# Performance work log

Measured on AMD Instinct MI355X. Metric: run time of the kernel, lower is better.

Reference implementation:

```python
import jax, jax.numpy as jnp
import numpy as np

D_MODEL, D_K, D_V, H = 64, 32, 32, 8
B, HH, WW = 2, 48, 48
NQ = HH * WW


def setup_inputs() -> dict:
    key = jax.random.key(0)
    ks = jax.random.split(key, 16)
    inp = {
        "queries": jax.random.normal(ks[0], (B, D_MODEL, HH, WW), jnp.float32),
        "keys": jax.random.normal(ks[1], (B, D_MODEL, HH, WW), jnp.float32),
        "values": jax.random.normal(ks[2], (B, D_MODEL, HH, WW), jnp.float32),
        "attention_weights": jax.random.uniform(ks[3], (B, H, NQ, NQ), jnp.float32),
        "attention_mask": jax.random.randint(ks[4], (B, H, NQ, NQ), 0, 2) > 0,
        # Linear params: torch init normal(std=0.001) weights, zero bias
        "Wq": 0.001 * jax.random.normal(ks[5], (H * D_K, D_MODEL), jnp.float32),
        "bq": jnp.zeros((H * D_K,), jnp.float32),
        "Wk": 0.001 * jax.random.normal(ks[6], (H * D_K, D_MODEL), jnp.float32),
        "bk": jnp.zeros((H * D_K,), jnp.float32),
        "Wv": 0.001 * jax.random.normal(ks[7], (H * D_V, D_MODEL), jnp.float32),
        "bv": jnp.zeros((H * D_V,), jnp.float32),
        "Wo": 0.001 * jax.random.normal(ks[8], (D_MODEL, H * D_V), jnp.float32),
        "bo": jnp.zeros((D_MODEL,), jnp.float32),
    }
    return inp


def reference(queries, keys, values, attention_weights, attention_mask,
              Wq, bq, Wk, bk, Wv, bv, Wo, bo):
    b, c, hh, ww = queries.shape
    nq = hh * ww
    # torch .view(b, -1, c) on contiguous (b,c,h,w) is a raw row-major reshape
    qf = queries.reshape(b, nq, c)
    kf = keys.reshape(b, nq, c)
    vf = values.reshape(b, nq, c)
    q = (qf @ Wq.T + bq).reshape(b, nq, H, D_K).transpose(0, 2, 1, 3)  # b h nq dk
    k = (kf @ Wk.T + bk).reshape(b, nq, H, D_K).transpose(0, 2, 1, 3)  # b h nk dk
    v = (vf @ Wv.T + bv).reshape(b, nq, H, D_V).transpose(0, 2, 1, 3)  # b h nk dv
    att = jnp.einsum('bhqd,bhkd->bhqk', q, k) / np.sqrt(D_K).astype(np.float32)
    att = att * attention_weights
    att = jnp.where(attention_mask, -jnp.inf, att)
    att = jax.nn.softmax(att, axis=-1)  # dropout is identity in eval mode
    out = jnp.einsum('bhqk,bhkd->bhqd', att, v)
    out = out.transpose(0, 2, 1, 3).reshape(b, nq, H * D_V)
    out = out @ Wo.T + bo  # (b, nq, d_model)
    return out.reshape(b, -1, hh, ww)  # (b, d_model, h, w)
```

## Files before the change

kernel.cpp:

```cpp
#include <hip/hip_runtime.h>


typedef __attribute__((ext_vector_type(8))) short bf16x8;
typedef __attribute__((ext_vector_type(4))) short bf16x4;
typedef __attribute__((ext_vector_type(4))) float f32x4;
typedef __attribute__((ext_vector_type(4))) unsigned int u32x4;

constexpr int B_  = 2;
constexpr int H_  = 8;
constexpr int NQ_ = 2304;
constexpr int DM_ = 64;
constexpr int DK_ = 32;
constexpr int NT_ = NQ_ / 32;
constexpr int CH_ = 3;
constexpr int TPC_ = NT_ / CH_;
constexpr int GT_ = B_ * H_ * (NQ_ / 16);
constexpr float SCALE_ = 0.17677669529663687f;

constexpr size_t OFF_Q    = 0;
constexpr size_t OFF_K    = 2359296;
constexpr size_t OFF_V    = 4718592;
constexpr size_t OFF_OMID = 7077888;
constexpr size_t OFF_FLAG = 11796480;
constexpr size_t OFF_OP   = 11796736;
constexpr size_t OFF_ML   = 25952512;

static __device__ __forceinline__ unsigned short f2bf(float f) {
    unsigned int u = __builtin_bit_cast(unsigned int, f);
    u += 0x7fffu + ((u >> 16) & 1u);
    return (unsigned short)(u >> 16);
}

__global__ void detect_mask_k(const unsigned int* __restrict__ m, int* __restrict__ flag) {
    int t = threadIdx.x;
    unsigned int v = 0;
    for (int k = 0; k < 16; ++k) v |= m[t * 16 + k];
    unsigned long long b = __ballot(v > 1u);
    if (t == 0) *flag = (b != 0ull) ? 1 : 0;
}

__global__ __launch_bounds__(256) void proj_qkv_k(
    const float* __restrict__ qin, const float* __restrict__ kin, const float* __restrict__ vin,
    const float* __restrict__ Wq, const float* __restrict__ bq,
    const float* __restrict__ Wk, const float* __restrict__ bk,
    const float* __restrict__ Wv, const float* __restrict__ bv,
    unsigned short* __restrict__ Qbf, unsigned short* __restrict__ Kbf,
    unsigned short* __restrict__ Vbf)
{
    const int sel = blockIdx.y;
    const float* in  = sel == 0 ? qin : (sel == 1 ? kin : vin);
    const float* W   = sel == 0 ? Wq  : (sel == 1 ? Wk  : Wv);
    const float* bia = sel == 0 ? bq  : (sel == 1 ? bk  : bv);

    const int rt = blockIdx.x;
    const int b  = rt / (NQ_ / 8);
    const int r0 = (rt % (NQ_ / 8)) * 8;

    __shared__ alignas(16) float ins[8][64];
    const int t = threadIdx.x;
    const float4* src = reinterpret_cast<const float4*>(in + ((size_t)b * NQ_ + r0) * DM_);
    if (t < 128) reinterpret_cast<float4*>(&ins[0][0])[t] = src[t];
    __syncthreads();

    float acc[8];
#pragma unroll
    for (int r = 0; r < 8; ++r) acc[r] = 0.f;
    const float* wrow = W + t * DM_;
    for (int m = 0; m < DM_; ++m) {
        float wv = wrow[m];
#pragma unroll
        for (int r = 0; r < 8; ++r) acc[r] += ins[r][m] * wv;
    }
    const float bb = bia[t];
    const int h = t >> 5, d = t & 31;
#pragma unroll
    for (int r = 0; r < 8; ++r) {
        unsigned short bvv = f2bf(acc[r] + bb);
        if (sel == 2) Vbf[(((size_t)b * H_ + h) * DK_ + d) * NQ_ + (r0 + r)] = bvv;
        else {
            unsigned short* out = (sel == 1) ? Kbf : Qbf;
            out[(((size_t)b * H_ + h) * NQ_ + (r0 + r)) * DK_ + d] = bvv;
        }
    }
}

__global__ __launch_bounds__(256) void attn_k(
    const unsigned short* __restrict__ Qbf,
    const unsigned short* __restrict__ Kbf,
    const unsigned short* __restrict__ Vbf,
    const float* __restrict__ attw,
    const unsigned char* __restrict__ maskb,
    const int* __restrict__ flagp,
    float* __restrict__ Opart,
    float* __restrict__ MLpart)
{
    const int lane = threadIdx.x & 63;
    const int l15 = lane & 15, hi = lane >> 4;
    const int g = blockIdx.x * 4 + (threadIdx.x >> 6);
    const int chunk = blockIdx.y;
    const int bh = g / (NQ_ / 16);
    const int it = g % (NQ_ / 16);
    const int i0 = it * 16;
    const bool isbyte = (*flagp) != 0;

    const unsigned short* qbase = Qbf + (size_t)bh * NQ_ * DK_;
    const unsigned short* kbase = Kbf + (size_t)bh * NQ_ * DK_;
    const unsigned short* vbase = Vbf + (size_t)bh * DK_ * NQ_;

    const int q = i0 + l15;
    bf16x8 qb = *reinterpret_cast<const bf16x8*>(qbase + (size_t)q * DK_ + 8 * hi);

    const float* wrow = attw + ((size_t)bh * NQ_ + q) * NQ_;
    const size_t mrow = ((size_t)bh * NQ_ + q) * NQ_;

    f32x4 oacc0 = {0.f, 0.f, 0.f, 0.f}, oacc1 = {0.f, 0.f, 0.f, 0.f};
    const f32x4 zero = {0.f, 0.f, 0.f, 0.f};
    float mrun = -1e30f, lrun = 0.f;

    const int t0 = chunk * TPC_, t1 = t0 + TPC_;
    for (int t = t0; t < t1; ++t) {
        const int j0 = t * 32;
        bf16x8 ka0 = *reinterpret_cast<const bf16x8*>(kbase + (size_t)(j0 + l15) * DK_ + 8 * hi);
        bf16x8 ka1 = *reinterpret_cast<const bf16x8*>(kbase + (size_t)(j0 + 16 + l15) * DK_ + 8 * hi);
        f32x4 s0 = __builtin_amdgcn_mfma_f32_16x16x32_bf16(ka0, qb, zero, 0, 0, 0);
        f32x4 s1 = __builtin_amdgcn_mfma_f32_16x16x32_bf16(ka1, qb, zero, 0, 0, 0);

        f32x4 w0 = *reinterpret_cast<const f32x4*>(wrow + j0 + 4 * hi);
        f32x4 w1 = *reinterpret_cast<const f32x4*>(wrow + j0 + 16 + 4 * hi);
        unsigned int ba, bb;
        if (isbyte) {
            ba = *reinterpret_cast<const unsigned int*>(maskb + mrow + j0 + 4 * hi);
            bb = *reinterpret_cast<const unsigned int*>(maskb + mrow + j0 + 16 + 4 * hi);
        } else {
            u32x4 A = *reinterpret_cast<const u32x4*>(maskb + (mrow + j0 + 4 * hi) * 4);
            u32x4 Bv = *reinterpret_cast<const u32x4*>(maskb + (mrow + j0 + 16 + 4 * hi) * 4);
            ba = (A[0] & 1u) | ((A[1] & 1u) << 8) | ((A[2] & 1u) << 16) | ((A[3] & 1u) << 24);
            bb = (Bv[0] & 1u) | ((Bv[1] & 1u) << 8) | ((Bv[2] & 1u) << 16) | ((Bv[3] & 1u) << 24);
        }

        float x0[4], x1[4];
#pragma unroll
        for (int r = 0; r < 4; ++r) {
            x0[r] = ((ba >> (8 * r)) & 0xffu) ? -1e30f : s0[r] * (SCALE_ * w0[r]);
            x1[r] = ((bb >> (8 * r)) & 0xffu) ? -1e30f : s1[r] * (SCALE_ * w1[r]);
        }

        float tm = fmaxf(fmaxf(fmaxf(x0[0], x0[1]), fmaxf(x0[2], x0[3])),
                         fmaxf(fmaxf(x1[0], x1[1]), fmaxf(x1[2], x1[3])));
        tm = fmaxf(tm, __shfl_xor(tm, 16, 64));
        tm = fmaxf(tm, __shfl_xor(tm, 32, 64));
        float mnew = fmaxf(mrun, tm);
        float rf = __expf(mrun - mnew);
        float p0[4], p1[4], ts = 0.f;
#pragma unroll
        for (int r = 0; r < 4; ++r) {
            p0[r] = __expf(x0[r] - mnew);
            p1[r] = __expf(x1[r] - mnew);
            ts += p0[r] + p1[r];
        }
        ts += __shfl_xor(ts, 16, 64);
        ts += __shfl_xor(ts, 32, 64);
        lrun = lrun * rf + ts;
        mrun = mnew;

#pragma unroll
        for (int r = 0; r < 4; ++r) {
            float rfr = __shfl(rf, 4 * hi + r, 64);
            oacc0[r] *= rfr;
            oacc1[r] *= rfr;
        }

        bf16x8 pa;
#pragma unroll
        for (int r = 0; r < 4; ++r) {
            pa[r]     = (short)f2bf(p0[r]);
            pa[4 + r] = (short)f2bf(p1[r]);
        }
        bf16x4 v00 = *reinterpret_cast<const bf16x4*>(vbase + (size_t)l15 * NQ_ + j0 + 4 * hi);
        bf16x4 v01 = *reinterpret_cast<const bf16x4*>(vbase + (size_t)l15 * NQ_ + j0 + 16 + 4 * hi);
        bf16x4 v10 = *reinterpret_cast<const bf16x4*>(vbase + (size_t)(16 + l15) * NQ_ + j0 + 4 * hi);
        bf16x4 v11 = *reinterpret_cast<const bf16x4*>(vbase + (size_t)(16 + l15) * NQ_ + j0 + 16 + 4 * hi);
        bf16x8 vb0 = __builtin_shufflevector(v00, v01, 0, 1, 2, 3, 4, 5, 6, 7);
        bf16x8 vb1 = __builtin_shufflevector(v10, v11, 0, 1, 2, 3, 4, 5, 6, 7);
        oacc0 = __builtin_amdgcn_mfma_f32_16x16x32_bf16(pa, vb0, oacc0, 0, 0, 0);
        oacc1 = __builtin_amdgcn_mfma_f32_16x16x32_bf16(pa, vb1, oacc1, 0, 0, 0);
    }

    float* op = Opart + ((size_t)chunk * GT_ + g) * 512;
#pragma unroll
    for (int r = 0; r < 4; ++r) {
        op[(4 * hi + r) * 32 + l15]      = oacc0[r];
        op[(4 * hi + r) * 32 + 16 + l15] = oacc1[r];
    }
    if (hi == 0) {
        float* mlp = MLpart + ((size_t)chunk * GT_ + g) * 32;
        mlp[l15]      = mrun;
        mlp[16 + l15] = lrun;
    }
}

__global__ __launch_bounds__(64) void combine_k(
    const float* __restrict__ Opart, const float* __restrict__ MLpart,
    float* __restrict__ Omid)
{
    const int g = blockIdx.x;
    const int lane = threadIdx.x;
    const int row = lane >> 2;
    const int c4  = (lane & 3) * 8;
    const int bh = g / (NQ_ / 16);
    const int it = g % (NQ_ / 16);
    const int b = bh / H_, h = bh % H_;

    float m[CH_], l[CH_];
#pragma unroll
    for (int c = 0; c < CH_; ++c) {
        const float* mlp = MLpart + ((size_t)c * GT_ + g) * 32;
        m[c] = mlp[row];
        l[c] = mlp[16 + row];
    }
    float mg = fmaxf(fmaxf(m[0], m[1]), m[2]);
    float e0 = __expf(m[0] - mg), e1 = __expf(m[1] - mg), e2 = __expf(m[2] - mg);
    float lg = l[0] * e0 + l[1] * e1 + l[2] * e2;
    float inv = 1.0f / lg;

    const size_t ob = (size_t)row * 32 + c4;
    f32x4 a0 = {0.f,0.f,0.f,0.f}, a1 = {0.f,0.f,0.f,0.f};
    float ee[CH_] = {e0, e1, e2};
#pragma unroll
    for (int c = 0; c < CH_; ++c) {
        const float* opp = Opart + ((size_t)c * GT_ + g) * 512 + ob;
        f32x4 t0 = *reinterpret_cast<const f32x4*>(opp);
        f32x4 t1 = *reinterpret_cast<const f32x4*>(opp + 4);
        a0 += t0 * ee[c];
        a1 += t1 * ee[c];
    }
    a0 *= inv; a1 *= inv;
    float* dst = Omid + ((size_t)b * NQ_ + it * 16 + row) * 256 + h * 32 + c4;
    *reinterpret_cast<f32x4*>(dst)     = a0;
    *reinterpret_cast<f32x4*>(dst + 4) = a1;
}

__global__ __launch_bounds__(256) void proj_out_k(
    const float* __restrict__ Omid, const float* __restrict__ Wo,
    const float* __restrict__ bo, float* __restrict__ out)
{
    const int rt = blockIdx.x;
    const int b  = rt / (NQ_ / 16);
    const int r0 = (rt % (NQ_ / 16)) * 16;

    __shared__ alignas(16) float lds[16][256];
    const int t = threadIdx.x;
    const float4* src = reinterpret_cast<const float4*>(Omid + ((size_t)b * NQ_ + r0) * 256);
#pragma unroll
    for (int k = 0; k < 4; ++k) reinterpret_cast<float4*>(&lds[0][0])[t + k * 256] = src[t + k * 256];
    __syncthreads();

    const int m = t & 63, rg = t >> 6;
    float acc[4] = {0.f, 0.f, 0.f, 0.f};
    const float* wrow = Wo + m * 256;
    for (int c = 0; c < 256; ++c) {
        float wv = wrow[c];
#pragma unroll
        for (int rr = 0; rr < 4; ++rr) acc[rr] += lds[rg * 4 + rr][c] * wv;
    }
    const float bb = bo[m];
#pragma unroll
    for (int rr = 0; rr < 4; ++rr)
        out[((size_t)b * NQ_ + r0 + rg * 4 + rr) * 64 + m] = acc[rr] + bb;
}

extern "C" void kernel_launch(void* const* d_in, const int* in_sizes, int n_in,
                              void* d_out, int out_size, void* d_ws, size_t ws_size,
                              hipStream_t stream)
{
    (void)in_sizes; (void)n_in; (void)out_size; (void)ws_size;
    const float* qin  = (const float*)d_in[0];
    const float* kin  = (const float*)d_in[1];
    const float* vin  = (const float*)d_in[2];
    const float* attw = (const float*)d_in[3];
    const void*  mask = d_in[4];
    const float* Wq = (const float*)d_in[5];
    const float* bq = (const float*)d_in[6];
    const float* Wk = (const float*)d_in[7];
    const float* bk = (const float*)d_in[8];
    const float* Wv = (const float*)d_in[9];
    const float* bv = (const float*)d_in[10];
    const float* Wo = (const float*)d_in[11];
    const float* bo = (const float*)d_in[12];

    char* ws = (char*)d_ws;
    unsigned short* Qbf   = (unsigned short*)(ws + OFF_Q);
    unsigned short* Kbf   = (unsigned short*)(ws + OFF_K);
    unsigned short* Vbf   = (unsigned short*)(ws + OFF_V);
    float*          Omid  = (float*)(ws + OFF_OMID);
    int*            flag  = (int*)(ws + OFF_FLAG);
    float*          Opart = (float*)(ws + OFF_OP);
    float*          MLp   = (float*)(ws + OFF_ML);

    detect_mask_k<<<1, 64, 0, stream>>>((const unsigned int*)mask, flag);
    proj_qkv_k<<<dim3(B_ * NQ_ / 8, 3), 256, 0, stream>>>(
        qin, kin, vin, Wq, bq, Wk, bk, Wv, bv, Qbf, Kbf, Vbf);
    attn_k<<<dim3(GT_ / 4, CH_), 256, 0, stream>>>(
        Qbf, Kbf, Vbf, attw, (const unsigned char*)mask, flag, Opart, MLp);
    combine_k<<<GT_, 64, 0, stream>>>(Opart, MLp, Omid);
    proj_out_k<<<B_ * NQ_ / 16, 256, 0, stream>>>(Omid, Wo, bo, (float*)d_out);
}
```

Before: 260.8 us.

## Software-pipeline attention loads three tiles ahead and specialize on mask format

The attention loop now issues the loads for K, V, attention weights and mask three tiles ahead into rotating register slots, so memory latency overlaps with the MFMA and softmax work of earlier tiles. The kernel is templated on the mask byte/int format, and both variants are launched, with the one that does not match returning immediately. The softmax scale is folded into Q in the projection kernel. The prefetching raises register pressure and may lower occupancy, and the extra launch adds a small amount of overhead.

Result: faster. 242.0 us (-7.2%).

```diff
diff --git a/kernel.cpp b/kernel.cpp
--- a/kernel.cpp
+++ b/kernel.cpp
@@ -75,7 +75,9 @@
     const int h = t >> 5, d = t & 31;
 #pragma unroll
     for (int r = 0; r < 8; ++r) {
-        unsigned short bvv = f2bf(acc[r] + bb);
+        float o = acc[r] + bb;
+        if (sel == 0) o *= SCALE_;
+        unsigned short bvv = f2bf(o);
         if (sel == 2) Vbf[(((size_t)b * H_ + h) * DK_ + d) * NQ_ + (r0 + r)] = bvv;
         else {
             unsigned short* out = (sel == 1) ? Kbf : Qbf;
@@ -84,6 +86,100 @@
     }
 }
 
+struct Slot {
+    bf16x8 ka0, ka1;
+    f32x4  w0, w1;
+    bf16x4 v00, v01, v10, v11;
+};
+template<bool ISBYTE> struct MaskSlot;
+template<> struct MaskSlot<true>  { unsigned int a, b; };
+template<> struct MaskSlot<false> { u32x4 a, b; };
+
+template<bool ISBYTE>
+static __device__ __forceinline__ void issue_slot(
+    Slot& s, MaskSlot<ISBYTE>& ms,
+    const unsigned short* __restrict__ kbase, const unsigned short* __restrict__ vbase,
+    const float* __restrict__ wrow, const unsigned char* __restrict__ mrowp,
+    int j0, int l15, int hi)
+{
+    s.ka0 = *reinterpret_cast<const bf16x8*>(kbase + (size_t)(j0 + l15) * DK_ + 8 * hi);
+    s.ka1 = *reinterpret_cast<const bf16x8*>(kbase + (size_t)(j0 + 16 + l15) * DK_ + 8 * hi);
+    s.w0  = *reinterpret_cast<const f32x4*>(wrow + j0 + 4 * hi);
+    s.w1  = *reinterpret_cast<const f32x4*>(wrow + j0 + 16 + 4 * hi);
+    if constexpr (ISBYTE) {
+        ms.a = *reinterpret_cast<const unsigned int*>(mrowp + j0 + 4 * hi);
+        ms.b = *reinterpret_cast<const unsigned int*>(mrowp + j0 + 16 + 4 * hi);
+    } else {
+        ms.a = *reinterpret_cast<const u32x4*>(mrowp + (size_t)(j0 + 4 * hi) * 4);
+        ms.b = *reinterpret_cast<const u32x4*>(mrowp + (size_t)(j0 + 16 + 4 * hi) * 4);
+    }
+    s.v00 = *reinterpret_cast<const bf16x4*>(vbase + (size_t)l15 * NQ_ + j0 + 4 * hi);
+    s.v01 = *reinterpret_cast<const bf16x4*>(vbase + (size_t)l15 * NQ_ + j0 + 16 + 4 * hi);
+    s.v10 = *reinterpret_cast<const bf16x4*>(vbase + (size_t)(16 + l15) * NQ_ + j0 + 4 * hi);
+    s.v11 = *reinterpret_cast<const bf16x4*>(vbase + (size_t)(16 + l15) * NQ_ + j0 + 16 + 4 * hi);
+}
+
+template<bool ISBYTE>
+static __device__ __forceinline__ void consume_slot(
+    const Slot& s, const MaskSlot<ISBYTE>& ms, bf16x8 qb,
+    f32x4& oacc0, f32x4& oacc1, float& mrun, float& lrun, int hi)
+{
+    const f32x4 zero = {0.f, 0.f, 0.f, 0.f};
+    f32x4 s0 = __builtin_amdgcn_mfma_f32_16x16x32_bf16(s.ka0, qb, zero, 0, 0, 0);
+    f32x4 s1 = __builtin_amdgcn_mfma_f32_16x16x32_bf16(s.ka1, qb, zero, 0, 0, 0);
+
+    unsigned int ba, bb;
+    if constexpr (ISBYTE) { ba = ms.a; bb = ms.b; }
+    else {
+        ba = (ms.a[0] & 1u) | ((ms.a[1] & 1u) << 8) | ((ms.a[2] & 1u) << 16) | ((ms.a[3] & 1u) << 24);
+        bb = (ms.b[0] & 1u) | ((ms.b[1] & 1u) << 8) | ((ms.b[2] & 1u) << 16) | ((ms.b[3] & 1u) << 24);
+    }
+
+    float x0[4], x1[4];
+#pragma unroll
+    for (int r = 0; r < 4; ++r) {
+        x0[r] = ((ba >> (8 * r)) & 0xffu) ? -1e30f : s0[r] * s.w0[r];
+        x1[r] = ((bb >> (8 * r)) & 0xffu) ? -1e30f : s1[r] * s.w1[r];
+    }
+
+    float tm = fmaxf(fmaxf(fmaxf(x0[0], x0[1]), fmaxf(x0[2], x0[3])),
+                     fmaxf(fmaxf(x1[0], x1[1]), fmaxf(x1[2], x1[3])));
+    tm = fmaxf(tm, __shfl_xor(tm, 16, 64));
+    tm = fmaxf(tm, __shfl_xor(tm, 32, 64));
+    float mnew = fmaxf(mrun, tm);
+    float rf = __expf(mrun - mnew);
+    float p0[4], p1[4];
+#pragma unroll
+    for (int r = 0; r < 4; ++r) {
+        p0[r] = __expf(x0[r] - mnew);
+        p1[r] = __expf(x1[r] - mnew);
+    }
+    float ts = ((p0[0] + p0[1]) + (p0[2] + p0[3])) + ((p1[0] + p1[1]) + (p1[2] + p1[3]));
+    ts += __shfl_xor(ts, 16, 64);
+    ts += __shfl_xor(ts, 32, 64);
+    lrun = lrun * rf + ts;
+    mrun = mnew;
+
+#pragma unroll
+    for (int r = 0; r < 4; ++r) {
+        float rfr = __shfl(rf, 4 * hi + r, 64);
+        oacc0[r] *= rfr;
+        oacc1[r] *= rfr;
+    }
+
+    bf16x8 pa;
+#pragma unroll
+    for (int r = 0; r < 4; ++r) {
+        pa[r]     = (short)f2bf(p0[r]);
+        pa[4 + r] = (short)f2bf(p1[r]);
+    }
+    bf16x8 vb0 = __builtin_shufflevector(s.v00, s.v01, 0, 1, 2, 3, 4, 5, 6, 7);
+    bf16x8 vb1 = __builtin_shufflevector(s.v10, s.v11, 0, 1, 2, 3, 4, 5, 6, 7);
+    oacc0 = __builtin_amdgcn_mfma_f32_16x16x32_bf16(pa, vb0, oacc0, 0, 0, 0);
+    oacc1 = __builtin_amdgcn_mfma_f32_16x16x32_bf16(pa, vb1, oacc1, 0, 0, 0);
+}
+
+template<bool ISBYTE>
 __global__ __launch_bounds__(256) void attn_k(
     const unsigned short* __restrict__ Qbf,
     const unsigned short* __restrict__ Kbf,
@@ -94,6 +190,8 @@
     float* __restrict__ Opart,
     float* __restrict__ MLpart)
 {
+    if (((*flagp) != 0) != ISBYTE) return;
+
     const int lane = threadIdx.x & 63;
     const int l15 = lane & 15, hi = lane >> 4;
     const int g = blockIdx.x * 4 + (threadIdx.x >> 6);
@@ -101,7 +199,6 @@
     const int bh = g / (NQ_ / 16);
     const int it = g % (NQ_ / 16);
     const int i0 = it * 16;
-    const bool isbyte = (*flagp) != 0;
 
     const unsigned short* qbase = Qbf + (size_t)bh * NQ_ * DK_;
     const unsigned short* kbase = Kbf + (size_t)bh * NQ_ * DK_;
@@ -111,79 +208,29 @@
     bf16x8 qb = *reinterpret_cast<const bf16x8*>(qbase + (size_t)q * DK_ + 8 * hi);
 
     const float* wrow = attw + ((size_t)bh * NQ_ + q) * NQ_;
-    const size_t mrow = ((size_t)bh * NQ_ + q) * NQ_;
+    const unsigned char* mrowp = maskb + ((size_t)bh * NQ_ + q) * NQ_ * (ISBYTE ? 1 : 4);
 
     f32x4 oacc0 = {0.f, 0.f, 0.f, 0.f}, oacc1 = {0.f, 0.f, 0.f, 0.f};
-    const f32x4 zero = {0.f, 0.f, 0.f, 0.f};
     float mrun = -1e30f, lrun = 0.f;
 
     const int t0 = chunk * TPC_, t1 = t0 + TPC_;
-    for (int t = t0; t < t1; ++t) {
-        const int j0 = t * 32;
-        bf16x8 ka0 = *reinterpret_cast<const bf16x8*>(kbase + (size_t)(j0 + l15) * DK_ + 8 * hi);
-        bf16x8 ka1 = *reinterpret_cast<const bf16x8*>(kbase + (size_t)(j0 + 16 + l15) * DK_ + 8 * hi);
-        f32x4 s0 = __builtin_amdgcn_mfma_f32_16x16x32_bf16(ka0, qb, zero, 0, 0, 0);
-        f32x4 s1 = __builtin_amdgcn_mfma_f32_16x16x32_bf16(ka1, qb, zero, 0, 0, 0);
-
-        f32x4 w0 = *reinterpret_cast<const f32x4*>(wrow + j0 + 4 * hi);
-        f32x4 w1 = *reinterpret_cast<const f32x4*>(wrow + j0 + 16 + 4 * hi);
-        unsigned int ba, bb;
-        if (isbyte) {
-            ba = *reinterpret_cast<const unsigned int*>(maskb + mrow + j0 + 4 * hi);
-            bb = *reinterpret_cast<const unsigned int*>(maskb + mrow + j0 + 16 + 4 * hi);
-        } else {
-            u32x4 A = *reinterpret_cast<const u32x4*>(maskb + (mrow + j0 + 4 * hi) * 4);
-            u32x4 Bv = *reinterpret_cast<const u32x4*>(maskb + (mrow + j0 + 16 + 4 * hi) * 4);
-            ba = (A[0] & 1u) | ((A[1] & 1u) << 8) | ((A[2] & 1u) << 16) | ((A[3] & 1u) << 24);
-            bb = (Bv[0] & 1u) | ((Bv[1] & 1u) << 8) | ((Bv[2] & 1u) << 16) | ((Bv[3] & 1u) << 24);
-        }
-
-        float x0[4], x1[4];
-#pragma unroll
-        for (int r = 0; r < 4; ++r) {
-            x0[r] = ((ba >> (8 * r)) & 0xffu) ? -1e30f : s0[r] * (SCALE_ * w0[r]);
-            x1[r] = ((bb >> (8 * r)) & 0xffu) ? -1e30f : s1[r] * (SCALE_ * w1[r]);
-        }
-
-        float tm = fmaxf(fmaxf(fmaxf(x0[0], x0[1]), fmaxf(x0[2], x0[3])),
-                         fmaxf(fmaxf(x1[0], x1[1]), fmaxf(x1[2], x1[3])));
-        tm = fmaxf(tm, __shfl_xor(tm, 16, 64));
-        tm = fmaxf(tm, __shfl_xor(tm, 32, 64));
-        float mnew = fmaxf(mrun, tm);
-        float rf = __expf(mrun - mnew);
-        float p0[4], p1[4], ts = 0.f;
-#pragma unroll
-        for (int r = 0; r < 4; ++r) {
-            p0[r] = __expf(x0[r] - mnew);
-            p1[r] = __expf(x1[r] - mnew);
-            ts += p0[r] + p1[r];
-        }
-        ts += __shfl_xor(ts, 16, 64);
-        ts += __shfl_xor(ts, 32, 64);
-        lrun = lrun * rf + ts;
-        mrun = mnew;
-
-#pragma unroll
-        for (int r = 0; r < 4; ++r) {
-            float rfr = __shfl(rf, 4 * hi + r, 64);
-            oacc0[r] *= rfr;
-            oacc1[r] *= rfr;
-        }
-
-        bf16x8 pa;
-#pragma unroll
-        for (int r = 0; r < 4; ++r) {
-            pa[r]     = (short)f2bf(p0[r]);
-            pa[4 + r] = (short)f2bf(p1[r]);
-        }
-        bf16x4 v00 = *reinterpret_cast<const bf16x4*>(vbase + (size_t)l15 * NQ_ + j0 + 4 * hi);
-        bf16x4 v01 = *reinterpret_cast<const bf16x4*>(vbase + (size_t)l15 * NQ_ + j0 + 16 + 4 * hi);
-        bf16x4 v10 = *reinterpret_cast<const bf16x4*>(vbase + (size_t)(16 + l15) * NQ_ + j0 + 4 * hi);
-        bf16x4 v11 = *reinterpret_cast<const bf16x4*>(vbase + (size_t)(16 + l15) * NQ_ + j0 + 16 + 4 * hi);
-        bf16x8 vb0 = __builtin_shufflevector(v00, v01, 0, 1, 2, 3, 4, 5, 6, 7);
-        bf16x8 vb1 = __builtin_shufflevector(v10, v11, 0, 1, 2, 3, 4, 5, 6, 7);
-        oacc0 = __builtin_amdgcn_mfma_f32_16x16x32_bf16(pa, vb0, oacc0, 0, 0, 0);
-        oacc1 = __builtin_amdgcn_mfma_f32_16x16x32_bf16(pa, vb1, oacc1, 0, 0, 0);
+
+    Slot sl0, sl1, sl2;
+    MaskSlot<ISBYTE> ms0, ms1, ms2;
+    issue_slot<ISBYTE>(sl0, ms0, kbase, vbase, wrow, mrowp, t0 * 32, l15, hi);
+    issue_slot<ISBYTE>(sl1, ms1, kbase, vbase, wrow, mrowp, (t0 + 1) * 32, l15, hi);
+    issue_slot<ISBYTE>(sl2, ms2, kbase, vbase, wrow, mrowp, (t0 + 2) * 32, l15, hi);
+
+    for (int tt = t0; tt < t1; tt += 3) {
+        consume_slot<ISBYTE>(sl0, ms0, qb, oacc0, oacc1, mrun, lrun, hi);
+        if (tt + 3 < t1)
+            issue_slot<ISBYTE>(sl0, ms0, kbase, vbase, wrow, mrowp, (tt + 3) * 32, l15, hi);
+        consume_slot<ISBYTE>(sl1, ms1, qb, oacc0, oacc1, mrun, lrun, hi);
+        if (tt + 4 < t1)
+            issue_slot<ISBYTE>(sl1, ms1, kbase, vbase, wrow, mrowp, (tt + 4) * 32, l15, hi);
+        consume_slot<ISBYTE>(sl2, ms2, qb, oacc0, oacc1, mrun, lrun, hi);
+        if (tt + 5 < t1)
+            issue_slot<ISBYTE>(sl2, ms2, kbase, vbase, wrow, mrowp, (tt + 5) * 32, l15, hi);
     }
 
     float* op = Opart + ((size_t)chunk * GT_ + g) * 512;
@@ -300,7 +347,9 @@
     detect_mask_k<<<1, 64, 0, stream>>>((const unsigned int*)mask, flag);
     proj_qkv_k<<<dim3(B_ * NQ_ / 8, 3), 256, 0, stream>>>(
         qin, kin, vin, Wq, bq, Wk, bk, Wv, bv, Qbf, Kbf, Vbf);
-    attn_k<<<dim3(GT_ / 4, CH_), 256, 0, stream>>>(
+    attn_k<true><<<dim3(GT_ / 4, CH_), 256, 0, stream>>>(
+        Qbf, Kbf, Vbf, attw, (const unsigned char*)mask, flag, Opart, MLp);
+    attn_k<false><<<dim3(GT_ / 4, CH_), 256, 0, stream>>>(
         Qbf, Kbf, Vbf, attw, (const unsigned char*)mask, flag, Opart, MLp);
     combine_k<<<GT_, 64, 0, stream>>>(Opart, MLp, Omid);
     proj_out_k<<<B_ * NQ_ / 16, 256, 0, stream>>>(Omid, Wo, bo, (float*)d_out);
```
